# Kernel optimization log

Hardware: AMD Instinct MI355X
Metric: run time of the kernel (lower is better)

Reference implementation:

```python
import jax, jax.numpy as jnp
import numpy as np

N_NODES = 50000
N_EDGES = 1600000
IN_FEATS = 128
HIDDEN = 16
HEADS = 8
SLOPE = 0.2


def setup_inputs() -> dict:
    key = jax.random.key(0)
    ks = jax.random.split(key, 9)
    feat = jax.random.normal(ks[0], (N_NODES, IN_FEATS), dtype=jnp.float32)
    edge_src = jax.random.randint(ks[1], (N_EDGES,), 0, N_NODES, dtype=jnp.int32)
    edge_dst = jax.random.randint(ks[2], (N_EDGES,), 0, N_NODES, dtype=jnp.int32)
    # layer 0: in=128 -> H*F=128 ; layer 1: in=128 (concat of layer 0) -> 128
    s0 = 1.0 / np.sqrt(IN_FEATS)
    W0 = jax.random.normal(ks[3], (IN_FEATS, HEADS * HIDDEN), dtype=jnp.float32) * s0
    al0 = jax.random.normal(ks[4], (HEADS, HIDDEN), dtype=jnp.float32) * 0.1
    ar0 = jax.random.normal(ks[5], (HEADS, HIDDEN), dtype=jnp.float32) * 0.1
    W1 = jax.random.normal(ks[6], (HEADS * HIDDEN, HEADS * HIDDEN), dtype=jnp.float32) * s0
    al1 = jax.random.normal(ks[7], (HEADS, HIDDEN), dtype=jnp.float32) * 0.1
    ar1 = jax.random.normal(ks[8], (HEADS, HIDDEN), dtype=jnp.float32) * 0.1
    return {"feat": feat, "edge_src": edge_src, "edge_dst": edge_dst,
            "W0": W0, "al0": al0, "ar0": ar0, "W1": W1, "al1": al1, "ar1": ar1}


def _gat_conv(feat, W, al, ar, src, dst):
    """One DGL-style GATConv: no bias, no residual, no dropout, no activation."""
    n = feat.shape[0]
    h = (feat @ W).reshape(n, HEADS, HIDDEN)              # [N,H,F]
    el = jnp.sum(h * al, axis=-1)                          # [N,H]
    er = jnp.sum(h * ar, axis=-1)                          # [N,H]
    e = jax.nn.leaky_relu(el[src] + er[dst], negative_slope=SLOPE)  # [E,H]
    # edge softmax over incoming edges of each dst node
    m = jax.ops.segment_max(e, dst, num_segments=n)        # [N,H]
    ex = jnp.exp(e - m[dst])                               # [E,H]
    denom = jax.ops.segment_sum(ex, dst, num_segments=n)   # [N,H]
    alpha = ex / jnp.where(denom[dst] > 0, denom[dst], 1.0)
    # message passing: gather src features, weight, scatter-add to dst
    out = jax.ops.segment_sum(h[src] * alpha[:, :, None], dst, num_segments=n)
    return out                                             # [N,H,F]


def reference(feat, edge_src, edge_dst, W0, al0, ar0, W1, al1, ar1):
    n = feat.shape[0]
    # step 1 + concat (flatten heads)
    x = _gat_conv(feat, W0, al0, ar0, edge_src, edge_dst).reshape(n, HEADS * HIDDEN)
    # step 2 + concat
    x = _gat_conv(x, W1, al1, ar1, edge_src, edge_dst).reshape(n, HEADS * HIDDEN)
    return x
```

## Files before the change

kernel.cpp:

```cpp
#include <hip/hip_runtime.h>
#include <hip/hip_bf16.h>


#define HEADS 8
#define HID 16
#define HF 128
#define SLOPE 0.2f

#define BSHIFT 8
#define BRANGE 256
#define CHUNK 4096


__global__ __launch_bounds__(512) void bucket_hist_kernel(
    const int* __restrict__ dst, int* __restrict__ bcount, int E, int nb) {
    __shared__ int h[BRANGE];
    int t = threadIdx.x;
    if (t < BRANGE) h[t] = 0;
    __syncthreads();
    int base = blockIdx.x * CHUNK;
    int end = base + CHUNK; if (end > E) end = E;
    for (int i = base + t; i < end; i += 512)
        atomicAdd(&h[dst[i] >> BSHIFT], 1);
    __syncthreads();
    if (t < nb && h[t]) atomicAdd(&bcount[t], h[t]);
}

__global__ __launch_bounds__(256) void bucket_scan_kernel(
    const int* __restrict__ bcount, int* __restrict__ bbase,
    int* __restrict__ gcur, int* __restrict__ rowptr, int nb, int N, int E) {
    __shared__ int s[256];
    int t = threadIdx.x;
    s[t] = (t < nb) ? bcount[t] : 0;
    __syncthreads();
    #pragma unroll
    for (int off = 1; off < 256; off <<= 1) {
        int v = (t >= off) ? s[t - off] : 0;
        __syncthreads();
        s[t] += v;
        __syncthreads();
    }
    int excl = (t == 0) ? 0 : s[t - 1];
    if (t < nb) { bbase[t] = excl; gcur[t] = excl; }
    if (t == 0) { bbase[nb] = E; rowptr[N] = E; }
}

__global__ __launch_bounds__(512) void bucket_scatter_kernel(
    const int* __restrict__ src, const int* __restrict__ dst,
    int* __restrict__ gcur, int* __restrict__ stage, int E, int nb) {
    __shared__ int hist[BRANGE];
    __shared__ int lscan[BRANGE];
    __shared__ int lcur[BRANGE];
    __shared__ int boff[BRANGE];
    __shared__ int sstage[CHUNK];
    int t = threadIdx.x;
    if (t < BRANGE) hist[t] = 0;
    __syncthreads();
    int base = blockIdx.x * CHUNK;
    int end = base + CHUNK; if (end > E) end = E;

    for (int i = base + t; i < end; i += 512)
        atomicAdd(&hist[dst[i] >> BSHIFT], 1);
    __syncthreads();

    if (t < 256) lscan[t] = hist[t];
    __syncthreads();
    #pragma unroll
    for (int off = 1; off < 256; off <<= 1) {
        int v = 0;
        if (t < 256 && t >= off) v = lscan[t - off];
        __syncthreads();
        if (t < 256) lscan[t] += v;
        __syncthreads();
    }
    int ex = 0;
    if (t < 256) ex = (t == 0) ? 0 : lscan[t - 1];
    __syncthreads();
    if (t < 256) {
        lcur[t] = ex;
        lscan[t] = ex;
        if (t < nb && hist[t] > 0) boff[t] = atomicAdd(&gcur[t], hist[t]);
    }
    __syncthreads();

    for (int i = base + t; i < end; i += 512) {
        int d = dst[i];
        int b = d >> BSHIFT;
        int pos = atomicAdd(&lcur[b], 1);
        sstage[pos] = (src[i] & 0xFFFF) | ((d & (BRANGE - 1)) << 16) | (b << 24);
    }
    __syncthreads();

    int total = end - base;
    for (int i = t; i < total; i += 512) {
        int p = sstage[i];
        int b = ((unsigned)p) >> 24;
        int gpos = boff[b] + (i - lscan[b]);
        stage[gpos] = p;
    }
}

__global__ __launch_bounds__(512) void bucket_csr_kernel(
    const int* __restrict__ stage, const int* __restrict__ bbase,
    int* __restrict__ rowptr, int* __restrict__ col, int N, int nb) {
    __shared__ int hist[BRANGE];
    __shared__ int lscan[BRANGE];
    __shared__ int lcur[BRANGE];
    int b = blockIdx.x;
    int t = threadIdx.x;
    int e0 = bbase[b], e1 = bbase[b + 1];
    if (t < BRANGE) hist[t] = 0;
    __syncthreads();
    for (int i = e0 + t; i < e1; i += 512)
        atomicAdd(&hist[(stage[i] >> 16) & (BRANGE - 1)], 1);
    __syncthreads();
    if (t < 256) lscan[t] = hist[t];
    __syncthreads();
    #pragma unroll
    for (int off = 1; off < 256; off <<= 1) {
        int v = 0;
        if (t < 256 && t >= off) v = lscan[t - off];
        __syncthreads();
        if (t < 256) lscan[t] += v;
        __syncthreads();
    }
    if (t < 256) {
        int ex = (t == 0) ? 0 : lscan[t - 1];
        lcur[t] = ex;
        int node = (b << BSHIFT) + t;
        if (node < N) rowptr[node] = e0 + ex;
    }
    __syncthreads();
    for (int i = e0 + t; i < e1; i += 512) {
        int p = stage[i];
        int pos = e0 + atomicAdd(&lcur[(p >> 16) & (BRANGE - 1)], 1);
        col[pos] = p & 0xFFFF;
    }
}


static __device__ __forceinline__ unsigned short f2bf(float f) {
    unsigned int u = __float_as_uint(f);
    u += 0x7fffu + ((u >> 16) & 1u);
    return (unsigned short)(u >> 16);
}

__global__ __launch_bounds__(256) void gemm_elr_kernel(
    const float* __restrict__ X, const float* __restrict__ W,
    const float* __restrict__ AL, const float* __restrict__ AR,
    unsigned short* __restrict__ Hb, float* __restrict__ EL,
    float* __restrict__ ER, int n) {
    __shared__ float xs[64][128];
    int t = threadIdx.x;
    int row0 = blockIdx.x * 64;
    int validRows = n - row0; if (validRows > 64) validRows = 64;

    const float4* Xv = (const float4*)(X + (size_t)row0 * HF);
    int nv = validRows * 32;
    for (int i = t; i < nv; i += 256)
        ((float4*)xs)[i] = Xv[i];
    __syncthreads();

    int c0 = (t & 31) * 4;
    int r0 = (t >> 5) * 8;
    float acc[8][4] = {};
    #pragma unroll 4
    for (int k = 0; k < 128; ++k) {
        float4 wv = *(const float4*)(W + k * HF + c0);
        #pragma unroll
        for (int i = 0; i < 8; ++i) {
            float x = xs[r0 + i][k];
            acc[i][0] += x * wv.x;
            acc[i][1] += x * wv.y;
            acc[i][2] += x * wv.z;
            acc[i][3] += x * wv.w;
        }
    }

    float4 alv = *(const float4*)(AL + c0);
    float4 arv = *(const float4*)(AR + c0);
    int head = (t & 31) >> 2;

    #pragma unroll
    for (int i = 0; i < 8; ++i) {
        int r = row0 + r0 + i;
        float el = acc[i][0] * alv.x + acc[i][1] * alv.y + acc[i][2] * alv.z + acc[i][3] * alv.w;
        float er = acc[i][0] * arv.x + acc[i][1] * arv.y + acc[i][2] * arv.z + acc[i][3] * arv.w;
        el += __shfl_xor(el, 1); el += __shfl_xor(el, 2);
        er += __shfl_xor(er, 1); er += __shfl_xor(er, 2);
        if (r < n) {
            ushort4 hb = make_ushort4(f2bf(acc[i][0]), f2bf(acc[i][1]),
                                      f2bf(acc[i][2]), f2bf(acc[i][3]));
            *(ushort4*)(Hb + (size_t)r * HF + c0) = hb;
            if ((t & 3) == 0) {
                EL[r * HEADS + head] = el;
                ER[r * HEADS + head] = er;
            }
        }
    }
}


__global__ __launch_bounds__(256) void gat_aggregate_kernel(
    const unsigned int* __restrict__ HbU,
    const float* __restrict__ EL, const float* __restrict__ ER,
    const int* __restrict__ rowptr, const int* __restrict__ col,
    float* __restrict__ OUT, int n) {
    int wid = (int)((blockIdx.x * blockDim.x + threadIdx.x) >> 6);
    if (wid >= n) return;
    int lane = threadIdx.x & 63;
    int s0 = rowptr[wid], s1 = rowptr[wid + 1];
    size_t ob = (size_t)wid * HF;
    if (s1 == s0) {
        ((float2*)(OUT + ob))[lane] = make_float2(0.f, 0.f);
        return;
    }

    int h = lane & 7;
    int j = lane >> 3;
    int hC = lane >> 3;
    float er_h = ER[wid * HEADS + h];

    float accx = 0.f, accy = 0.f;
    float dpart = 0.f;

    for (int base = s0; base < s1; base += 8) {
        int i = base + j;
        int icl = i < s1 ? i : s1 - 1;
        int sj = col[icl];
        float e = EL[sj * HEADS + h] + er_h;
        e = fmaxf(e, SLOPE * e);
        float w = __expf(e);
        if (i >= s1) w = 0.f;
        dpart += w;

        if (base + 8 <= s1) {
            #pragma unroll
            for (int jj = 0; jj < 8; ++jj) {
                float wC = __shfl(w, jj * 8 + hC);
                int s = __builtin_amdgcn_readlane(sj, jj * 8);
                unsigned int pv = HbU[(size_t)s * 64 + lane];
                accx += wC * __uint_as_float(pv << 16);
                accy += wC * __uint_as_float(pv & 0xffff0000u);
            }
        } else {
            int ne = s1 - base;
            for (int jj = 0; jj < ne; ++jj) {
                float wC = __shfl(w, jj * 8 + hC);
                int s = __builtin_amdgcn_readlane(sj, jj * 8);
                unsigned int pv = HbU[(size_t)s * 64 + lane];
                accx += wC * __uint_as_float(pv << 16);
                accy += wC * __uint_as_float(pv & 0xffff0000u);
            }
        }
    }

    dpart += __shfl_xor(dpart, 8);
    dpart += __shfl_xor(dpart, 16);
    dpart += __shfl_xor(dpart, 32);
    float rC = 1.f / __shfl(dpart, hC);

    ((float2*)(OUT + ob))[lane] = make_float2(accx * rC, accy * rC);
}


extern "C" void kernel_launch(void* const* d_in, const int* in_sizes, int n_in,
                              void* d_out, int out_size, void* d_ws, size_t ws_size,
                              hipStream_t stream) {
    const float* feat = (const float*)d_in[0];
    const int*   esrc = (const int*)d_in[1];
    const int*   edst = (const int*)d_in[2];
    const float* W0   = (const float*)d_in[3];
    const float* al0  = (const float*)d_in[4];
    const float* ar0  = (const float*)d_in[5];
    const float* W1   = (const float*)d_in[6];
    const float* al1  = (const float*)d_in[7];
    const float* ar1  = (const float*)d_in[8];
    float* out = (float*)d_out;

    const int N = in_sizes[0] / HF;
    const int E = in_sizes[1];
    const int nb = (N + BRANGE - 1) >> BSHIFT;

    char* w = (char*)d_ws;
    auto alloc = [&](size_t bytes) -> void* {
        void* p = (void*)w;
        w += (bytes + 255) & ~(size_t)255;
        return p;
    };
    unsigned short* hb = (unsigned short*)alloc((size_t)N * HF * 2);
    float* x1     = (float*)alloc((size_t)N * HF * 4);
    float* el_buf = (float*)alloc((size_t)N * HEADS * 4);
    float* er_buf = (float*)alloc((size_t)N * HEADS * 4);
    int*   rowptr = (int*)alloc((size_t)(N + 1) * 4);
    int*   col    = (int*)alloc((size_t)E * 4);
    int*   bcount = (int*)alloc((size_t)nb * 4);
    int*   bbase  = (int*)alloc((size_t)(nb + 1) * 4);
    int*   gcur   = (int*)alloc((size_t)nb * 4);
    int*   stage  = (int*)x1;

    hipMemsetAsync(bcount, 0, (size_t)nb * 4, stream);
    int gChunk = (E + CHUNK - 1) / CHUNK;
    bucket_hist_kernel<<<gChunk, 512, 0, stream>>>(edst, bcount, E, nb);
    bucket_scan_kernel<<<1, 256, 0, stream>>>(bcount, bbase, gcur, rowptr, nb, N, E);
    bucket_scatter_kernel<<<gChunk, 512, 0, stream>>>(esrc, edst, gcur, stage, E, nb);
    bucket_csr_kernel<<<nb, 512, 0, stream>>>(stage, bbase, rowptr, col, N, nb);

    int gGemm = (N + 63) / 64;
    int gAgg  = (N * 64 + 255) / 256;

    gemm_elr_kernel<<<gGemm, 256, 0, stream>>>(feat, W0, al0, ar0, hb, el_buf, er_buf, N);
    gat_aggregate_kernel<<<gAgg, 256, 0, stream>>>((const unsigned int*)hb, el_buf, er_buf,
                                                   rowptr, col, x1, N);

    gemm_elr_kernel<<<gGemm, 256, 0, stream>>>(x1, W1, al1, ar1, hb, el_buf, er_buf, N);
    gat_aggregate_kernel<<<gAgg, 256, 0, stream>>>((const unsigned int*)hb, el_buf, er_buf,
                                                   rowptr, col, out, N);
}
```

Measured before the change: 255.7 us.

## Replace FP32 FMA GEMM with bf16 MFMA GEMM using pre-transposed weights

Adds a small kernel that transposes and converts W0/W1 to bf16 once per call. The dense projection now converts X to bf16 in swizzled LDS and computes with 16x16x32 bf16 MFMA instructions instead of scalar FP32 FMAs. EL/ER are computed from the MFMA accumulators with cross-lane shuffles. This cuts GEMM compute time but lowers input precision to bf16 and adds two tiny launches.

```diff
diff --git a/kernel.cpp b/kernel.cpp
--- a/kernel.cpp
+++ b/kernel.cpp
@@ -10,6 +10,15 @@
 #define BSHIFT 8
 #define BRANGE 256
 #define CHUNK 4096
+
+typedef __attribute__((ext_vector_type(8))) short bf16x8;
+typedef __attribute__((ext_vector_type(4))) float f32x4;
+
+static __device__ __forceinline__ unsigned int f2bf(float f) {
+    unsigned int u = __float_as_uint(f);
+    u += 0x7fffu + ((u >> 16) & 1u);
+    return u >> 16;
+}
 
 
 __global__ __launch_bounds__(512) void bucket_hist_kernel(
@@ -139,63 +148,137 @@
 }
 
 
-static __device__ __forceinline__ unsigned short f2bf(float f) {
-    unsigned int u = __float_as_uint(f);
-    u += 0x7fffu + ((u >> 16) & 1u);
-    return (unsigned short)(u >> 16);
-}
-
-__global__ __launch_bounds__(256) void gemm_elr_kernel(
-    const float* __restrict__ X, const float* __restrict__ W,
+__global__ __launch_bounds__(256) void wtrans_kernel(const float* __restrict__ W,
+                                                     unsigned short* __restrict__ Wtb) {
+    int gid = blockIdx.x * 256 + threadIdx.x;
+    int c = gid >> 3;
+    int k0 = (gid & 7) * 16;
+    #pragma unroll
+    for (int q = 0; q < 4; ++q) {
+        int k = k0 + q * 4;
+        ushort4 o = make_ushort4(
+            (unsigned short)f2bf(W[(k + 0) * HF + c]),
+            (unsigned short)f2bf(W[(k + 1) * HF + c]),
+            (unsigned short)f2bf(W[(k + 2) * HF + c]),
+            (unsigned short)f2bf(W[(k + 3) * HF + c]));
+        *(ushort4*)(Wtb + (size_t)c * HF + k) = o;
+    }
+}
+
+
+__global__ __launch_bounds__(256) void gemm_mfma_kernel(
+    const float* __restrict__ X, const unsigned short* __restrict__ Wtb,
     const float* __restrict__ AL, const float* __restrict__ AR,
     unsigned short* __restrict__ Hb, float* __restrict__ EL,
     float* __restrict__ ER, int n) {
-    __shared__ float xs[64][128];
+    __shared__ __align__(16) unsigned short xs[64 * HF];
+    __shared__ __align__(16) unsigned short ws[HF * HF];
     int t = threadIdx.x;
     int row0 = blockIdx.x * 64;
-    int validRows = n - row0; if (validRows > 64) validRows = 64;
-
-    const float4* Xv = (const float4*)(X + (size_t)row0 * HF);
-    int nv = validRows * 32;
-    for (int i = t; i < nv; i += 256)
-        ((float4*)xs)[i] = Xv[i];
-    __syncthreads();
-
-    int c0 = (t & 31) * 4;
-    int r0 = (t >> 5) * 8;
-    float acc[8][4] = {};
-    #pragma unroll 4
-    for (int k = 0; k < 128; ++k) {
-        float4 wv = *(const float4*)(W + k * HF + c0);
+
+    {
+        int r = t >> 2;
+        int k0 = (t & 3) * 32;
+        int gr = row0 + r;
+        float4 f[8];
+        if (gr < n) {
+            const float4* p = (const float4*)(X + (size_t)gr * HF + k0);
+            #pragma unroll
+            for (int i = 0; i < 8; ++i) f[i] = p[i];
+        } else {
+            #pragma unroll
+            for (int i = 0; i < 8; ++i) f[i] = make_float4(0.f, 0.f, 0.f, 0.f);
+        }
+        unsigned int rowbase = r * 256;
+        unsigned int sw = (r & 7) << 4;
+        #pragma unroll
+        for (int g2 = 0; g2 < 4; ++g2) {
+            float4 a = f[g2 * 2], b = f[g2 * 2 + 1];
+            int4 pk;
+            pk.x = (int)(f2bf(a.x) | (f2bf(a.y) << 16));
+            pk.y = (int)(f2bf(a.z) | (f2bf(a.w) << 16));
+            pk.z = (int)(f2bf(b.x) | (f2bf(b.y) << 16));
+            pk.w = (int)(f2bf(b.z) | (f2bf(b.w) << 16));
+            unsigned int addr = rowbase + ((unsigned)((k0 + g2 * 8) * 2) ^ sw);
+            *(int4*)((char*)xs + addr) = pk;
+        }
+    }
+    {
+        int c = t >> 1;
+        unsigned int kb0 = (t & 1) * 128;
+        const int4* src = (const int4*)((const char*)Wtb + (size_t)c * 256 + kb0);
+        unsigned int sw = (c & 7) << 4;
         #pragma unroll
         for (int i = 0; i < 8; ++i) {
-            float x = xs[r0 + i][k];
-            acc[i][0] += x * wv.x;
-            acc[i][1] += x * wv.y;
-            acc[i][2] += x * wv.z;
-            acc[i][3] += x * wv.w;
-        }
-    }
-
-    float4 alv = *(const float4*)(AL + c0);
-    float4 arv = *(const float4*)(AR + c0);
-    int head = (t & 31) >> 2;
-
-    #pragma unroll
-    for (int i = 0; i < 8; ++i) {
-        int r = row0 + r0 + i;
-        float el = acc[i][0] * alv.x + acc[i][1] * alv.y + acc[i][2] * alv.z + acc[i][3] * alv.w;
-        float er = acc[i][0] * arv.x + acc[i][1] * arv.y + acc[i][2] * arv.z + acc[i][3] * arv.w;
-        el += __shfl_xor(el, 1); el += __shfl_xor(el, 2);
-        er += __shfl_xor(er, 1); er += __shfl_xor(er, 2);
-        if (r < n) {
-            ushort4 hb = make_ushort4(f2bf(acc[i][0]), f2bf(acc[i][1]),
-                                      f2bf(acc[i][2]), f2bf(acc[i][3]));
-            *(ushort4*)(Hb + (size_t)r * HF + c0) = hb;
-            if ((t & 3) == 0) {
-                EL[r * HEADS + head] = el;
-                ER[r * HEADS + head] = er;
-            }
+            int4 v = src[i];
+            unsigned int addr = c * 256 + ((kb0 + i * 16) ^ sw);
+            *(int4*)((char*)ws + addr) = v;
+        }
+    }
+    __syncthreads();
+
+    int wv = t >> 6;
+    int l = t & 63;
+    int lr = l & 15;
+    int g = l >> 4;
+
+    bf16x8 bfr[4];
+    {
+        int r = wv * 16 + lr;
+        unsigned int rowbase = r * 256;
+        unsigned int sw = (r & 7) << 4;
+        #pragma unroll
+        for (int s = 0; s < 4; ++s) {
+            unsigned int kbyte = (unsigned)((s * 32 + g * 8) * 2);
+            bfr[s] = *(bf16x8*)((char*)xs + rowbase + (kbyte ^ sw));
+        }
+    }
+
+    f32x4 acc[8];
+    #pragma unroll
+    for (int ct = 0; ct < 8; ++ct) acc[ct] = (f32x4){0.f, 0.f, 0.f, 0.f};
+
+    #pragma unroll
+    for (int ct = 0; ct < 8; ++ct) {
+        int c = ct * 16 + lr;
+        unsigned int rowbase = c * 256;
+        unsigned int sw = (c & 7) << 4;
+        #pragma unroll
+        for (int s = 0; s < 4; ++s) {
+            unsigned int kbyte = (unsigned)((s * 32 + g * 8) * 2);
+            bf16x8 af = *(bf16x8*)((char*)ws + rowbase + (kbyte ^ sw));
+            acc[ct] = __builtin_amdgcn_mfma_f32_16x16x32_bf16(af, bfr[s], acc[ct], 0, 0, 0);
+        }
+    }
+
+    int grow = row0 + wv * 16 + lr;
+    bool valid = grow < n;
+
+    if (valid) {
+        #pragma unroll
+        for (int ct = 0; ct < 8; ++ct) {
+            ushort4 hb4 = make_ushort4(
+                (unsigned short)f2bf(acc[ct][0]), (unsigned short)f2bf(acc[ct][1]),
+                (unsigned short)f2bf(acc[ct][2]), (unsigned short)f2bf(acc[ct][3]));
+            *(ushort4*)(Hb + (size_t)grow * HF + ct * 16 + g * 4) = hb4;
+        }
+    }
+
+    #pragma unroll
+    for (int ct = 0; ct < 8; ++ct) {
+        float e1 = 0.f, e2 = 0.f;
+        #pragma unroll
+        for (int rg = 0; rg < 4; ++rg) {
+            float alv = AL[ct * 16 + g * 4 + rg];
+            float arv = AR[ct * 16 + g * 4 + rg];
+            e1 += acc[ct][rg] * alv;
+            e2 += acc[ct][rg] * arv;
+        }
+        e1 += __shfl_xor(e1, 16); e1 += __shfl_xor(e1, 32);
+        e2 += __shfl_xor(e2, 16); e2 += __shfl_xor(e2, 32);
+        if (g == 0 && valid) {
+            EL[grow * HEADS + ct] = e1;
+            ER[grow * HEADS + ct] = e2;
         }
     }
 }
@@ -288,7 +371,7 @@
         w += (bytes + 255) & ~(size_t)255;
         return p;
     };
-    unsigned short* hb = (unsigned short*)alloc((size_t)N * HF * 2);
+    unsigned short* hb   = (unsigned short*)alloc((size_t)N * HF * 2);
     float* x1     = (float*)alloc((size_t)N * HF * 4);
     float* el_buf = (float*)alloc((size_t)N * HEADS * 4);
     float* er_buf = (float*)alloc((size_t)N * HEADS * 4);
@@ -297,7 +380,12 @@
     int*   bcount = (int*)alloc((size_t)nb * 4);
     int*   bbase  = (int*)alloc((size_t)(nb + 1) * 4);
     int*   gcur   = (int*)alloc((size_t)nb * 4);
+    unsigned short* wtb0 = (unsigned short*)alloc((size_t)HF * HF * 2);
+    unsigned short* wtb1 = (unsigned short*)alloc((size_t)HF * HF * 2);
     int*   stage  = (int*)x1;
+
+    wtrans_kernel<<<4, 256, 0, stream>>>(W0, wtb0);
+    wtrans_kernel<<<4, 256, 0, stream>>>(W1, wtb1);
 
     hipMemsetAsync(bcount, 0, (size_t)nb * 4, stream);
     int gChunk = (E + CHUNK - 1) / CHUNK;
@@ -309,11 +397,11 @@
     int gGemm = (N + 63) / 64;
     int gAgg  = (N * 64 + 255) / 256;
 
-    gemm_elr_kernel<<<gGemm, 256, 0, stream>>>(feat, W0, al0, ar0, hb, el_buf, er_buf, N);
+    gemm_mfma_kernel<<<gGemm, 256, 0, stream>>>(feat, wtb0, al0, ar0, hb, el_buf, er_buf, N);
     gat_aggregate_kernel<<<gAgg, 256, 0, stream>>>((const unsigned int*)hb, el_buf, er_buf,
                                                    rowptr, col, x1, N);
 
-    gemm_elr_kernel<<<gGemm, 256, 0, stream>>>(x1, W1, al1, ar1, hb, el_buf, er_buf, N);
+    gemm_mfma_kernel<<<gGemm, 256, 0, stream>>>(x1, wtb1, al1, ar1, hb, el_buf, er_buf, N);
     gat_aggregate_kernel<<<gAgg, 256, 0, stream>>>((const unsigned int*)hb, el_buf, er_buf,
                                                    rowptr, col, out, N);
 }
```

Result: faster. 233.5 us (-8.7%).
